# Kernel tuning notes

Hardware: AMD Instinct MI355X
Metric: run time of the kernel (lower is better)

Reference implementation:

```python
import jax, jax.numpy as jnp
import numpy as np

H = 2048
L = 3  # conv_L_cache


def setup_inputs() -> dict:
    key = jax.random.key(0)
    k1, k2, k3, k4 = jax.random.split(key, 4)
    hidden_states = jax.random.normal(k1, (2, 4096, H), dtype=jnp.float32)
    W_in = jax.random.normal(k2, (3 * H, H), dtype=jnp.float32) * 0.02
    conv_w = jax.random.normal(k3, (H, 1, L), dtype=jnp.float32) * 0.1
    W_out = jax.random.normal(k4, (H, H), dtype=jnp.float32) * 0.02
    return {"hidden_states": hidden_states, "W_in": W_in, "conv_w": conv_w, "W_out": W_out}


def reference(hidden_states, W_in, conv_w, W_out):
    # in_proj: [b, s, H] @ [H, 3H] -> [b, s, 3H]
    BCx = jnp.einsum('bsh,gh->bsg', hidden_states, W_in)
    B, C, x = jnp.split(BCx, 3, axis=-1)  # each [b, s, H]
    Bx = (B * x).transpose(0, 2, 1)       # [b, H, s] pre-conv gating
    # depthwise causal conv1d, kernel L, left pad L-1 (== Conv1d pad L-1 then [:seqlen])
    conv_out = jax.lax.conv_general_dilated(
        Bx, conv_w,
        window_strides=(1,),
        padding=[(L - 1, 0)],
        feature_group_count=H,
        dimension_numbers=('NCH', 'OIH', 'NCH'),
    )  # [b, H, s]
    y = C.transpose(0, 2, 1) * conv_out   # post-conv gating, [b, H, s]
    y = y.transpose(0, 2, 1)              # [b, s, H]
    return jnp.einsum('bsh,oh->bso', y, W_out)
```

## Files before the change

kernel.cpp:

```cpp
#include <hip/hip_runtime.h>
#include <hip/hip_bf16.h>
#include <stdint.h>

typedef __bf16 bf16;
typedef __bf16 bf16x8 __attribute__((ext_vector_type(8)));
typedef float floatx4 __attribute__((ext_vector_type(4)));

#define BM 128
#define BN 256
#define BK 32

__global__ __launch_bounds__(256) void cast_f32_bf16(
    const float* __restrict__ in, bf16* __restrict__ out, int n)
{
    int i = (blockIdx.x * 256 + threadIdx.x) * 8;
    if (i >= n) return;
    float4 a = *(const float4*)(in + i);
    float4 b = *(const float4*)(in + i + 4);
    bf16x8 o;
    o[0] = (bf16)a.x; o[1] = (bf16)a.y; o[2] = (bf16)a.z; o[3] = (bf16)a.w;
    o[4] = (bf16)b.x; o[5] = (bf16)b.y; o[6] = (bf16)b.z; o[7] = (bf16)b.w;
    *(bf16x8*)(out + i) = o;
}

template <typename CT>
__global__ __launch_bounds__(256, 2) void gemm_bt(
    const bf16* __restrict__ A, const bf16* __restrict__ Bt, CT* __restrict__ C,
    int M, int N, int K)
{
    __shared__ __align__(16) bf16 As[2 * BM * BK];
    __shared__ __align__(16) bf16 Bs[2 * BN * BK];

    const int t  = threadIdx.x;
    const int w  = t >> 6;
    const int l  = t & 63;
    const int lq = l >> 4;
    const int lm = l & 15;
    const int wm = w & 1;
    const int wn = w >> 1;

    const int mBase = blockIdx.y * BM;
    const int nBase = blockIdx.x * BN;

    const int rowT  = t >> 2;
    const int lchnk = (t & 3) ^ ((t >> 3) & 3);
    const int kelm  = lchnk * 8;

    const bf16* gA0 = A  + (size_t)(mBase + rowT)       * K + kelm;
    const bf16* gA1 = A  + (size_t)(mBase + rowT + 64)  * K + kelm;
    const bf16* gB0 = Bt + (size_t)(nBase + rowT)       * K + kelm;
    const bf16* gB1 = Bt + (size_t)(nBase + rowT + 64)  * K + kelm;
    const bf16* gB2 = Bt + (size_t)(nBase + rowT + 128) * K + kelm;
    const bf16* gB3 = Bt + (size_t)(nBase + rowT + 192) * K + kelm;

    bf16* tA0 = As + t * 8;
    bf16* tA1 = As + 2048 + t * 8;
    bf16* tB0 = Bs + t * 8;
    bf16* tB1 = Bs + 2048 + t * 8;
    bf16* tB2 = Bs + 4096 + t * 8;
    bf16* tB3 = Bs + 6144 + t * 8;

    const int pc  = (lq ^ ((lm >> 1) & 3)) * 8;
    const int fAo = (wm * 64 + lm) * BK + pc;
    const int fBo = (wn * 128 + lm) * BK + pc;

    bf16x8 rA0 = *(const bf16x8*)(gA0);
    bf16x8 rA1 = *(const bf16x8*)(gA1);
    bf16x8 rB0 = *(const bf16x8*)(gB0);
    bf16x8 rB1 = *(const bf16x8*)(gB1);
    bf16x8 rB2 = *(const bf16x8*)(gB2);
    bf16x8 rB3 = *(const bf16x8*)(gB3);
    *(bf16x8*)(tA0) = rA0;
    *(bf16x8*)(tA1) = rA1;
    *(bf16x8*)(tB0) = rB0;
    *(bf16x8*)(tB1) = rB1;
    *(bf16x8*)(tB2) = rB2;
    *(bf16x8*)(tB3) = rB3;
    __syncthreads();

    floatx4 acc[4][8] = {};
    const int kIters = K / BK;

    for (int kk = 0; kk < kIters; ++kk) {
        const int curA = (kk & 1) * (BM * BK);
        const int curB = (kk & 1) * (BN * BK);
        const int nxtA = ((kk + 1) & 1) * (BM * BK);
        const int nxtB = ((kk + 1) & 1) * (BN * BK);
        const bool hasNext = (kk + 1 < kIters);

        if (hasNext) {
            const int off = (kk + 1) * BK;
            rA0 = *(const bf16x8*)(gA0 + off);
            rA1 = *(const bf16x8*)(gA1 + off);
            rB0 = *(const bf16x8*)(gB0 + off);
            rB1 = *(const bf16x8*)(gB1 + off);
            rB2 = *(const bf16x8*)(gB2 + off);
            rB3 = *(const bf16x8*)(gB3 + off);
        }

        bf16x8 a[4], b[8];
        #pragma unroll
        for (int i = 0; i < 4; ++i)
            a[i] = *(const bf16x8*)(As + curA + fAo + i * 16 * BK);
        #pragma unroll
        for (int j = 0; j < 8; ++j)
            b[j] = *(const bf16x8*)(Bs + curB + fBo + j * 16 * BK);
        #pragma unroll
        for (int i = 0; i < 4; ++i)
            #pragma unroll
            for (int j = 0; j < 8; ++j)
                acc[i][j] = __builtin_amdgcn_mfma_f32_16x16x32_bf16(a[i], b[j], acc[i][j], 0, 0, 0);

        if (hasNext) {
            *(bf16x8*)(tA0 + nxtA) = rA0;
            *(bf16x8*)(tA1 + nxtA) = rA1;
            *(bf16x8*)(tB0 + nxtB) = rB0;
            *(bf16x8*)(tB1 + nxtB) = rB1;
            *(bf16x8*)(tB2 + nxtB) = rB2;
            *(bf16x8*)(tB3 + nxtB) = rB3;
            __syncthreads();
        }
    }

    #pragma unroll
    for (int i = 0; i < 4; ++i) {
        #pragma unroll
        for (int j = 0; j < 8; ++j) {
            #pragma unroll
            for (int r = 0; r < 4; ++r) {
                const int row = mBase + wm * 64 + i * 16 + lq * 4 + r;
                const int col = nBase + wn * 128 + j * 16 + lm;
                C[(size_t)row * N + col] = (CT)acc[i][j][r];
            }
        }
    }
}

__global__ __launch_bounds__(256) void conv_gate(
    const bf16* __restrict__ BCx, const float* __restrict__ convw,
    bf16* __restrict__ Y)
{
    const int tx = threadIdx.x;
    const int h0 = tx * 8;
    const int bb = blockIdx.y;
    const int s0 = blockIdx.x * 32;

    float w0[8], w1[8], w2[8];
    #pragma unroll
    for (int j = 0; j < 8; ++j) {
        w0[j] = convw[(h0 + j) * 3 + 0];
        w1[j] = convw[(h0 + j) * 3 + 1];
        w2[j] = convw[(h0 + j) * 3 + 2];
    }

    const size_t mB = (size_t)bb * 4096;

    float bx1[8], bx2[8];
    #pragma unroll
    for (int j = 0; j < 8; ++j) { bx1[j] = 0.f; bx2[j] = 0.f; }
    if (s0 >= 2) {
        const bf16* r1 = BCx + (mB + s0 - 1) * 6144;
        const bf16* r2 = BCx + (mB + s0 - 2) * 6144;
        bf16x8 B1 = *(const bf16x8*)(r1 + h0);
        bf16x8 x1 = *(const bf16x8*)(r1 + 4096 + h0);
        bf16x8 B2 = *(const bf16x8*)(r2 + h0);
        bf16x8 x2 = *(const bf16x8*)(r2 + 4096 + h0);
        #pragma unroll
        for (int j = 0; j < 8; ++j) {
            bx1[j] = (float)B1[j] * (float)x1[j];
            bx2[j] = (float)B2[j] * (float)x2[j];
        }
    }

    for (int s = s0; s < s0 + 32; ++s) {
        const size_t m = mB + s;
        const bf16* rp = BCx + m * 6144;
        bf16x8 Bv = *(const bf16x8*)(rp + h0);
        bf16x8 Cv = *(const bf16x8*)(rp + 2048 + h0);
        bf16x8 xv = *(const bf16x8*)(rp + 4096 + h0);
        bf16x8 o;
        #pragma unroll
        for (int j = 0; j < 8; ++j) {
            float bx0 = (float)Bv[j] * (float)xv[j];
            float cv  = w0[j] * bx2[j] + w1[j] * bx1[j] + w2[j] * bx0;
            o[j] = (bf16)((float)Cv[j] * cv);
            bx2[j] = bx1[j];
            bx1[j] = bx0;
        }
        *(bf16x8*)(Y + m * 2048 + h0) = o;
    }
}

extern "C" void kernel_launch(void* const* d_in, const int* in_sizes, int n_in,
                              void* d_out, int out_size, void* d_ws, size_t ws_size,
                              hipStream_t stream) {
    const float* hidden = (const float*)d_in[0];
    const float* Win    = (const float*)d_in[1];
    const float* convw  = (const float*)d_in[2];
    const float* Wout   = (const float*)d_in[3];
    float* out = (float*)d_out;

    const int nH = 8192 * 2048;
    const int nWin = 6144 * 2048;
    const int nWout = 2048 * 2048;

    bf16* hB    = (bf16*)d_ws;
    bf16* WinB  = hB + (size_t)nH;
    bf16* WoutB = WinB + (size_t)nWin;
    bf16* BCx   = WoutB + (size_t)nWout;
    bf16* Y     = BCx + (size_t)8192 * 6144;

    cast_f32_bf16<<<nH / (256 * 8), 256, 0, stream>>>(hidden, hB, nH);
    cast_f32_bf16<<<nWin / (256 * 8), 256, 0, stream>>>(Win, WinB, nWin);
    cast_f32_bf16<<<nWout / (256 * 8), 256, 0, stream>>>(Wout, WoutB, nWout);

    gemm_bt<bf16><<<dim3(6144 / BN, 8192 / BM), dim3(256), 0, stream>>>(
        hB, WinB, BCx, 8192, 6144, 2048);
    conv_gate<<<dim3(4096 / 32, 2), dim3(256), 0, stream>>>(BCx, convw, Y);
    gemm_bt<float><<<dim3(2048 / BN, 8192 / BM), dim3(256), 0, stream>>>(
        Y, WoutB, out, 8192, 2048, 2048);
}
```

Before: 468.2 us.

## Rewrite GEMM with direct-to-LDS async loads, 4-stage pipeline, 32x32 MFMA

The bf16 GEMM is restructured to use 256x256 tiles with 512 threads (8 waves), 32x32x16 MFMA instructions, and a 4-deep LDS ring buffer filled by global_load_lds so global loads bypass registers. Explicit vmcnt waits and barriers let loads run three K-steps ahead of compute, and s_setprio raises wave priority around the MFMA block. This targets global-load latency and register pressure from staging through VGPRs. It uses 128KB of LDS per block, which may limit occupancy to one block per CU despite the launch bound of 2, and it relies on hand-placed waitcnt counts being correct.

```diff
diff --git a/kernel.cpp b/kernel.cpp
--- a/kernel.cpp
+++ b/kernel.cpp
@@ -4,11 +4,7 @@
 
 typedef __bf16 bf16;
 typedef __bf16 bf16x8 __attribute__((ext_vector_type(8)));
-typedef float floatx4 __attribute__((ext_vector_type(4)));
-
-#define BM 128
-#define BN 256
-#define BK 32
+typedef float floatx16 __attribute__((ext_vector_type(16)));
 
 __global__ __launch_bounds__(256) void cast_f32_bf16(
     const float* __restrict__ in, bf16* __restrict__ out, int n)
@@ -23,113 +19,122 @@
     *(bf16x8*)(out + i) = o;
 }
 
+__device__ __forceinline__ void load_lds16(const bf16* g, bf16* l) {
+    __builtin_amdgcn_global_load_lds(
+        (const __attribute__((address_space(1))) void*)g,
+        (__attribute__((address_space(3))) void*)l, 16, 0, 0);
+}
+
+#define VMCNT(N) asm volatile("s_waitcnt vmcnt(" #N ")" ::: "memory")
+
 template <typename CT>
-__global__ __launch_bounds__(256, 2) void gemm_bt(
+__global__ __launch_bounds__(512, 2) void gemm_bt(
     const bf16* __restrict__ A, const bf16* __restrict__ Bt, CT* __restrict__ C,
     int M, int N, int K)
 {
-    __shared__ __align__(16) bf16 As[2 * BM * BK];
-    __shared__ __align__(16) bf16 Bs[2 * BN * BK];
-
-    const int t  = threadIdx.x;
-    const int w  = t >> 6;
-    const int l  = t & 63;
-    const int lq = l >> 4;
-    const int lm = l & 15;
-    const int wm = w & 1;
-    const int wn = w >> 1;
-
-    const int mBase = blockIdx.y * BM;
-    const int nBase = blockIdx.x * BN;
-
-    const int rowT  = t >> 2;
-    const int lchnk = (t & 3) ^ ((t >> 3) & 3);
+    __shared__ __align__(16) bf16 As[4 * 8192];
+    __shared__ __align__(16) bf16 Bs[4 * 8192];
+
+    const int tid = threadIdx.x;
+    const int w     = tid >> 6;
+    const int l     = tid & 63;
+    const int wm    = w & 1;
+    const int wn    = w >> 1;
+    const int lm32  = l & 31;
+    const int lhalf = l >> 5;
+
+    const int mBase = blockIdx.y * 256;
+    const int nBase = blockIdx.x * 256;
+
+    const int rowT  = tid >> 2;
+    const int lchnk = (tid & 3) ^ ((tid >> 3) & 3);
     const int kelm  = lchnk * 8;
 
-    const bf16* gA0 = A  + (size_t)(mBase + rowT)       * K + kelm;
-    const bf16* gA1 = A  + (size_t)(mBase + rowT + 64)  * K + kelm;
-    const bf16* gB0 = Bt + (size_t)(nBase + rowT)       * K + kelm;
-    const bf16* gB1 = Bt + (size_t)(nBase + rowT + 64)  * K + kelm;
-    const bf16* gB2 = Bt + (size_t)(nBase + rowT + 128) * K + kelm;
-    const bf16* gB3 = Bt + (size_t)(nBase + rowT + 192) * K + kelm;
-
-    bf16* tA0 = As + t * 8;
-    bf16* tA1 = As + 2048 + t * 8;
-    bf16* tB0 = Bs + t * 8;
-    bf16* tB1 = Bs + 2048 + t * 8;
-    bf16* tB2 = Bs + 4096 + t * 8;
-    bf16* tB3 = Bs + 6144 + t * 8;
-
-    const int pc  = (lq ^ ((lm >> 1) & 3)) * 8;
-    const int fAo = (wm * 64 + lm) * BK + pc;
-    const int fBo = (wn * 128 + lm) * BK + pc;
-
-    bf16x8 rA0 = *(const bf16x8*)(gA0);
-    bf16x8 rA1 = *(const bf16x8*)(gA1);
-    bf16x8 rB0 = *(const bf16x8*)(gB0);
-    bf16x8 rB1 = *(const bf16x8*)(gB1);
-    bf16x8 rB2 = *(const bf16x8*)(gB2);
-    bf16x8 rB3 = *(const bf16x8*)(gB3);
-    *(bf16x8*)(tA0) = rA0;
-    *(bf16x8*)(tA1) = rA1;
-    *(bf16x8*)(tB0) = rB0;
-    *(bf16x8*)(tB1) = rB1;
-    *(bf16x8*)(tB2) = rB2;
-    *(bf16x8*)(tB3) = rB3;
-    __syncthreads();
-
-    floatx4 acc[4][8] = {};
-    const int kIters = K / BK;
-
-    for (int kk = 0; kk < kIters; ++kk) {
-        const int curA = (kk & 1) * (BM * BK);
-        const int curB = (kk & 1) * (BN * BK);
-        const int nxtA = ((kk + 1) & 1) * (BM * BK);
-        const int nxtB = ((kk + 1) & 1) * (BN * BK);
-        const bool hasNext = (kk + 1 < kIters);
-
-        if (hasNext) {
-            const int off = (kk + 1) * BK;
-            rA0 = *(const bf16x8*)(gA0 + off);
-            rA1 = *(const bf16x8*)(gA1 + off);
-            rB0 = *(const bf16x8*)(gB0 + off);
-            rB1 = *(const bf16x8*)(gB1 + off);
-            rB2 = *(const bf16x8*)(gB2 + off);
-            rB3 = *(const bf16x8*)(gB3 + off);
-        }
-
-        bf16x8 a[4], b[8];
-        #pragma unroll
-        for (int i = 0; i < 4; ++i)
-            a[i] = *(const bf16x8*)(As + curA + fAo + i * 16 * BK);
-        #pragma unroll
-        for (int j = 0; j < 8; ++j)
-            b[j] = *(const bf16x8*)(Bs + curB + fBo + j * 16 * BK);
-        #pragma unroll
-        for (int i = 0; i < 4; ++i)
-            #pragma unroll
-            for (int j = 0; j < 8; ++j)
-                acc[i][j] = __builtin_amdgcn_mfma_f32_16x16x32_bf16(a[i], b[j], acc[i][j], 0, 0, 0);
-
-        if (hasNext) {
-            *(bf16x8*)(tA0 + nxtA) = rA0;
-            *(bf16x8*)(tA1 + nxtA) = rA1;
-            *(bf16x8*)(tB0 + nxtB) = rB0;
-            *(bf16x8*)(tB1 + nxtB) = rB1;
-            *(bf16x8*)(tB2 + nxtB) = rB2;
-            *(bf16x8*)(tB3 + nxtB) = rB3;
-            __syncthreads();
-        }
-    }
+    const bf16* gA0 = A  + (size_t)(mBase + rowT) * K + kelm;
+    const bf16* gA1 = gA0 + (size_t)128 * K;
+    const bf16* gB0 = Bt + (size_t)(nBase + rowT) * K + kelm;
+    const bf16* gB1 = gB0 + (size_t)128 * K;
+
+    bf16* lA = As + tid * 8;
+    bf16* lB = Bs + tid * 8;
+
+    const int swz = (lm32 >> 1) & 3;
+    const int fA0 = (wm * 128 + lm32) * 32 + ((0 + lhalf) ^ swz) * 8;
+    const int fA1 = (wm * 128 + lm32) * 32 + ((2 + lhalf) ^ swz) * 8;
+    const int fB0 = (wn * 64  + lm32) * 32 + ((0 + lhalf) ^ swz) * 8;
+    const int fB1 = (wn * 64  + lm32) * 32 + ((2 + lhalf) ^ swz) * 8;
+
+#define STAGE(kt) do {                                   \
+        const int _b = ((kt) & 3) * 8192;                \
+        const int _o = (kt) * 32;                        \
+        load_lds16(gA0 + _o, lA + _b);                   \
+        load_lds16(gA1 + _o, lA + _b + 4096);            \
+        load_lds16(gB0 + _o, lB + _b);                   \
+        load_lds16(gB1 + _o, lB + _b + 4096);            \
+    } while (0)
+
+#define KSTEP(tt, NCNT) do {                                              \
+        VMCNT(NCNT);                                                      \
+        __builtin_amdgcn_s_barrier();                                     \
+        asm volatile("" ::: "memory");                                    \
+        __builtin_amdgcn_sched_barrier(0);                                \
+        const bf16* Ab = As + ((tt) & 3) * 8192;                          \
+        const bf16* Bb = Bs + ((tt) & 3) * 8192;                          \
+        bf16x8 a0[4], a1[4], b0[2], b1[2];                                \
+        _Pragma("unroll")                                                 \
+        for (int i = 0; i < 4; ++i) {                                     \
+            a0[i] = *(const bf16x8*)(Ab + fA0 + i * 1024);                \
+            a1[i] = *(const bf16x8*)(Ab + fA1 + i * 1024);                \
+        }                                                                 \
+        _Pragma("unroll")                                                 \
+        for (int j = 0; j < 2; ++j) {                                     \
+            b0[j] = *(const bf16x8*)(Bb + fB0 + j * 1024);                \
+            b1[j] = *(const bf16x8*)(Bb + fB1 + j * 1024);                \
+        }                                                                 \
+        __builtin_amdgcn_s_setprio(1);                                    \
+        _Pragma("unroll")                                                 \
+        for (int i = 0; i < 4; ++i)                                       \
+            _Pragma("unroll")                                             \
+            for (int j = 0; j < 2; ++j) {                                 \
+                acc[i][j] = __builtin_amdgcn_mfma_f32_32x32x16_bf16(      \
+                    a0[i], b0[j], acc[i][j], 0, 0, 0);                    \
+                acc[i][j] = __builtin_amdgcn_mfma_f32_32x32x16_bf16(      \
+                    a1[i], b1[j], acc[i][j], 0, 0, 0);                    \
+            }                                                             \
+        __builtin_amdgcn_s_setprio(0);                                    \
+        __builtin_amdgcn_sched_barrier(0);                                \
+        asm volatile("s_waitcnt lgkmcnt(0)" ::: "memory");                \
+        __builtin_amdgcn_sched_barrier(0);                                \
+        __builtin_amdgcn_s_barrier();                                     \
+        asm volatile("" ::: "memory");                                    \
+    } while (0)
+
+    floatx16 acc[4][2] = {};
+
+    STAGE(0); STAGE(1); STAGE(2);
+
+    const int kIters = K / 32;
+    int kt = 0;
+    for (; kt < kIters - 3; ++kt) {
+        STAGE(kt + 3);
+        KSTEP(kt, 12);
+    }
+    KSTEP(kt, 8); ++kt;
+    KSTEP(kt, 4); ++kt;
+    KSTEP(kt, 0);
+
+#undef STAGE
+#undef KSTEP
 
     #pragma unroll
     for (int i = 0; i < 4; ++i) {
         #pragma unroll
-        for (int j = 0; j < 8; ++j) {
+        for (int j = 0; j < 2; ++j) {
+            const int col = nBase + wn * 64 + j * 32 + lm32;
+            const int rB  = mBase + wm * 128 + i * 32 + 4 * lhalf;
             #pragma unroll
-            for (int r = 0; r < 4; ++r) {
-                const int row = mBase + wm * 64 + i * 16 + lq * 4 + r;
-                const int col = nBase + wn * 128 + j * 16 + lm;
+            for (int r = 0; r < 16; ++r) {
+                const int row = rB + (r & 3) + 8 * (r >> 2);
                 C[(size_t)row * N + col] = (CT)acc[i][j][r];
             }
         }
@@ -214,9 +219,9 @@
     cast_f32_bf16<<<nWin / (256 * 8), 256, 0, stream>>>(Win, WinB, nWin);
     cast_f32_bf16<<<nWout / (256 * 8), 256, 0, stream>>>(Wout, WoutB, nWout);
 
-    gemm_bt<bf16><<<dim3(6144 / BN, 8192 / BM), dim3(256), 0, stream>>>(
+    gemm_bt<bf16><<<dim3(6144 / 256, 8192 / 256), dim3(512), 0, stream>>>(
         hB, WinB, BCx, 8192, 6144, 2048);
     conv_gate<<<dim3(4096 / 32, 2), dim3(256), 0, stream>>>(BCx, convw, Y);
-    gemm_bt<float><<<dim3(2048 / BN, 8192 / BM), dim3(256), 0, stream>>>(
+    gemm_bt<float><<<dim3(2048 / 256, 8192 / 256), dim3(512), 0, stream>>>(
         Y, WoutB, out, 8192, 2048, 2048);
 }
```

After: 520.3 us. 11.1% more time.
